# Kernel tuning notes

Hardware: AMD Instinct MI355X
Metric: run time of the kernel (lower is better)

Reference implementation:

```python
import jax, jax.numpy as jnp
import numpy as np

def setup_inputs() -> dict:
    key = jax.random.key(0)
    k1, k2 = jax.random.split(key)
    N, M, D = 4096, 4096, 1024
    set1 = jax.random.normal(k1, (N, D), dtype=jnp.float32)
    set2 = jax.random.normal(k2, (M, D), dtype=jnp.float32)
    return {"set1": set1, "set2": set2}

def _l2_dist(x, y):
    # mean over D of squared differences, computed via the expanded GEMM form
    D = x.shape[-1]
    x2 = jnp.sum(x * x, axis=-1)          # [N]
    y2 = jnp.sum(y * y, axis=-1)          # [M]
    xy = jnp.einsum('nd,md->nm', x, y)    # [N, M]
    return (x2[:, None] - 2.0 * xy + y2[None, :]) / D

def reference(set1, set2):
    dist = _l2_dist(set1, set2)                 # [N, M]
    t1 = jnp.mean(jnp.min(dist, axis=1))        # nearest set2 point per set1 point
    t2 = jnp.mean(jnp.min(dist, axis=0))        # nearest set1 point per set2 point
    return (t1 + t2) * 0.5
```

## Files before the change

kernel.cpp:

```cpp
#include <hip/hip_runtime.h>
#include <hip/hip_bf16.h>
#include <stdint.h>


#define NPTS 4096
#define MPTS 4096
#define DDIM 1024

typedef __attribute__((ext_vector_type(8))) short bf16x8;
typedef __attribute__((ext_vector_type(4))) float f32x4;

__device__ __forceinline__ unsigned short f2bf(float f) {
    unsigned int u = __float_as_uint(f);
    unsigned int r = 0x7FFFu + ((u >> 16) & 1u);
    return (unsigned short)((u + r) >> 16);
}

__device__ __forceinline__ void gl_lds16(const void* g, void* l) {
    __builtin_amdgcn_global_load_lds(
        (const __attribute__((address_space(1))) unsigned int*)g,
        (__attribute__((address_space(3))) unsigned int*)l, 16, 0, 0);
}

__global__ __launch_bounds__(256) void prepass_kernel(
    const float* __restrict__ s1, const float* __restrict__ s2,
    unsigned short* __restrict__ b1, unsigned short* __restrict__ b2,
    float* __restrict__ norms ) {
    int row = blockIdx.x;
    const float* src;
    unsigned short* dst;
    if (row < NPTS) { src = s1 + (size_t)row * DDIM; dst = b1 + (size_t)row * DDIM; }
    else            { src = s2 + (size_t)(row - NPTS) * DDIM; dst = b2 + (size_t)(row - NPTS) * DDIM; }
    int t = threadIdx.x;
    float4 v = ((const float4*)src)[t];
    float sq = v.x * v.x + v.y * v.y + v.z * v.z + v.w * v.w;
    ushort4 o;
    o.x = f2bf(v.x); o.y = f2bf(v.y); o.z = f2bf(v.z); o.w = f2bf(v.w);
    ((ushort4*)dst)[t] = o;
    #pragma unroll
    for (int off = 32; off; off >>= 1) sq += __shfl_down(sq, off, 64);
    __shared__ float red[4];
    if ((t & 63) == 0) red[t >> 6] = sq;
    __syncthreads();
    if (t == 0) norms[row] = red[0] + red[1] + red[2] + red[3];
}

#define BM 128
#define BN 128
#define BK 64

__global__ __launch_bounds__(256) void cham_gemm_kernel(
    const unsigned short* __restrict__ A,
    const unsigned short* __restrict__ B,
    const float* __restrict__ x2, const float* __restrict__ y2,
    unsigned int* __restrict__ rowmin, unsigned int* __restrict__ colmin) {
    __shared__ unsigned short As[BM][BK];
    __shared__ unsigned short Bs[BN][BK];

    const int bid = blockIdx.x;
    const int bi = bid >> 5;
    const int bj = bid & 31;
    const int tid = threadIdx.x;
    const int wave = tid >> 6;
    const int lane = tid & 63;
    const int wr = wave >> 1;
    const int wc = wave & 1;

    f32x4 acc[4][4];
    #pragma unroll
    for (int i = 0; i < 4; ++i)
        #pragma unroll
        for (int j = 0; j < 4; ++j)
            acc[i][j] = (f32x4){0.f, 0.f, 0.f, 0.f};

    const unsigned short* Ab = A + (size_t)(bi * BM) * DDIM;
    const unsigned short* Bb = B + (size_t)(bj * BN) * DDIM;
    const char* AsB = (const char*)&As[0][0];
    const char* BsB = (const char*)&Bs[0][0];

    const int lr = lane >> 3;
    const int ch = lane & 7;

    for (int k0 = 0; k0 < DDIM; k0 += BK) {
        #pragma unroll
        for (int q = 0; q < 4; ++q) {
            int r = wave * 32 + q * 8 + lr;
            int sch = ch ^ (r & 7);
            gl_lds16(Ab + (size_t)r * DDIM + k0 + sch * 8, (void*)&As[wave * 32 + q * 8][0]);
            gl_lds16(Bb + (size_t)r * DDIM + k0 + sch * 8, (void*)&Bs[wave * 32 + q * 8][0]);
        }
        __syncthreads();

        #pragma unroll
        for (int kk = 0; kk < 2; ++kk) {
            const int kb = kk * 32 + (lane >> 4) * 8;
            bf16x8 af[4], bfr[4];
            #pragma unroll
            for (int fi = 0; fi < 4; ++fi) {
                int row = wr * 64 + fi * 16 + (lane & 15);
                int off = row * (BK * 2) + kb * 2;
                af[fi] = *(const bf16x8*)(AsB + (off ^ ((row & 7) << 4)));
            }
            #pragma unroll
            for (int fj = 0; fj < 4; ++fj) {
                int col = wc * 64 + fj * 16 + (lane & 15);
                int off = col * (BK * 2) + kb * 2;
                bfr[fj] = *(const bf16x8*)(BsB + (off ^ ((col & 7) << 4)));
            }
            #pragma unroll
            for (int fi = 0; fi < 4; ++fi)
                #pragma unroll
                for (int fj = 0; fj < 4; ++fj)
                    acc[fi][fj] = __builtin_amdgcn_mfma_f32_16x16x32_bf16(
                        af[fi], bfr[fj], acc[fi][fj], 0, 0, 0);
        }
        __syncthreads();
    }

    const float invD = 1.0f / (float)DDIM;
    const int nb = bi * BM + wr * 64;
    const int mb = bj * BN + wc * 64;

    float x2v[4][4];
    #pragma unroll
    for (int fi = 0; fi < 4; ++fi)
        #pragma unroll
        for (int rg = 0; rg < 4; ++rg)
            x2v[fi][rg] = x2[nb + fi * 16 + (lane >> 4) * 4 + rg];
    float y2v[4];
    #pragma unroll
    for (int fj = 0; fj < 4; ++fj)
        y2v[fj] = y2[mb + fj * 16 + (lane & 15)];

    float rv[4][4];
    float cv[4];
    #pragma unroll
    for (int fi = 0; fi < 4; ++fi)
        #pragma unroll
        for (int rg = 0; rg < 4; ++rg) rv[fi][rg] = 3.0e38f;
    #pragma unroll
    for (int fj = 0; fj < 4; ++fj) cv[fj] = 3.0e38f;

    #pragma unroll
    for (int fi = 0; fi < 4; ++fi)
        #pragma unroll
        for (int fj = 0; fj < 4; ++fj)
            #pragma unroll
            for (int rg = 0; rg < 4; ++rg) {
                float d = (x2v[fi][rg] + y2v[fj] - 2.0f * acc[fi][fj][rg]) * invD;
                rv[fi][rg] = fminf(rv[fi][rg], d);
                cv[fj] = fminf(cv[fj], d);
            }

    #pragma unroll
    for (int fi = 0; fi < 4; ++fi)
        #pragma unroll
        for (int rg = 0; rg < 4; ++rg) {
            float v = rv[fi][rg];
            v = fminf(v, __shfl_xor(v, 1, 64));
            v = fminf(v, __shfl_xor(v, 2, 64));
            v = fminf(v, __shfl_xor(v, 4, 64));
            v = fminf(v, __shfl_xor(v, 8, 64));
            if ((lane & 15) == 0) {
                int n = nb + fi * 16 + (lane >> 4) * 4 + rg;
                atomicMin(&rowmin[n], __float_as_uint(v));
            }
        }

    #pragma unroll
    for (int fj = 0; fj < 4; ++fj) {
        float v = cv[fj];
        v = fminf(v, __shfl_xor(v, 16, 64));
        v = fminf(v, __shfl_xor(v, 32, 64));
        if (lane < 16) {
            int m = mb + fj * 16 + lane;
            atomicMin(&colmin[m], __float_as_uint(v));
        }
    }
}

__global__ __launch_bounds__(1024) void finredux_kernel(
    const unsigned int* __restrict__ mins , float* __restrict__ out) {
    int t = threadIdx.x;
    float s = 0.f;
    #pragma unroll
    for (int i = 0; i < 8; ++i) s += __uint_as_float(mins[t + i * 1024]);
    #pragma unroll
    for (int off = 32; off; off >>= 1) s += __shfl_down(s, off, 64);
    __shared__ float ws_[16];
    if ((t & 63) == 0) ws_[t >> 6] = s;
    __syncthreads();
    if (t == 0) {
        float tot = 0.f;
        #pragma unroll
        for (int i = 0; i < 16; ++i) tot += ws_[i];
        out[0] = tot * (1.0f / 8192.0f);
    }
}

extern "C" void kernel_launch(void* const* d_in, const int* in_sizes, int n_in,
                              void* d_out, int out_size, void* d_ws, size_t ws_size,
                              hipStream_t stream) {
    const float* s1 = (const float*)d_in[0];
    const float* s2 = (const float*)d_in[1];
    char* ws = (char*)d_ws;

    unsigned short* b1 = (unsigned short*)ws;
    unsigned short* b2 = (unsigned short*)(ws + 8388608);
    float* norms       = (float*)(ws + 16777216);
    unsigned int* mins = (unsigned int*)(ws + 16777216 + 32768);
    float* out = (float*)d_out;

    hipMemsetAsync(mins, 0x7f, 32768, stream);

    prepass_kernel<<<NPTS + MPTS, 256, 0, stream>>>(s1, s2, b1, b2, norms);
    cham_gemm_kernel<<<(NPTS / BM) * (MPTS / BN), 256, 0, stream>>>(
        b1, b2, norms, norms + NPTS, mins, mins + NPTS);
    finredux_kernel<<<1, 1024, 0, stream>>>(mins, out);
}
```

Baseline: 130.9 us.

## Use 256x256 tiles with 4-slot async LDS pipeline and fold mins init into prepass

The GEMM moves from 128x128 tiles with 256 threads to 256x256 tiles with 512 threads (8 waves). A 4-slot, 128KB LDS ring buffer is filled by direct global-to-LDS loads issued several stages ahead, with explicit waitcnt, barriers and priority boosts around the MFMA blocks. This aims to hide load latency and raise arithmetic intensity, at the cost of only 256 blocks, which is about one per CU, and heavy register pressure. The prepass now handles one row per wave and initialises the min buffers itself, which removes the separate memset launch.

```diff
diff --git a/kernel.cpp b/kernel.cpp
--- a/kernel.cpp
+++ b/kernel.cpp
@@ -6,6 +6,7 @@
 #define NPTS 4096
 #define MPTS 4096
 #define DDIM 1024
+#define SLOTB 32768
 
 typedef __attribute__((ext_vector_type(8))) short bf16x8;
 typedef __attribute__((ext_vector_type(4))) float f32x4;
@@ -25,157 +26,171 @@
 __global__ __launch_bounds__(256) void prepass_kernel(
     const float* __restrict__ s1, const float* __restrict__ s2,
     unsigned short* __restrict__ b1, unsigned short* __restrict__ b2,
-    float* __restrict__ norms ) {
-    int row = blockIdx.x;
+    float* __restrict__ norms, unsigned int* __restrict__ mins) {
+    const int row = blockIdx.x * 4 + (threadIdx.x >> 6);
+    const int lane = threadIdx.x & 63;
     const float* src;
     unsigned short* dst;
     if (row < NPTS) { src = s1 + (size_t)row * DDIM; dst = b1 + (size_t)row * DDIM; }
     else            { src = s2 + (size_t)(row - NPTS) * DDIM; dst = b2 + (size_t)(row - NPTS) * DDIM; }
-    int t = threadIdx.x;
-    float4 v = ((const float4*)src)[t];
-    float sq = v.x * v.x + v.y * v.y + v.z * v.z + v.w * v.w;
-    ushort4 o;
-    o.x = f2bf(v.x); o.y = f2bf(v.y); o.z = f2bf(v.z); o.w = f2bf(v.w);
-    ((ushort4*)dst)[t] = o;
+    float sq = 0.f;
+    #pragma unroll
+    for (int i = 0; i < 4; ++i) {
+        float4 v = ((const float4*)src)[lane + i * 64];
+        sq += v.x * v.x + v.y * v.y + v.z * v.z + v.w * v.w;
+        ushort4 o;
+        o.x = f2bf(v.x); o.y = f2bf(v.y); o.z = f2bf(v.z); o.w = f2bf(v.w);
+        ((ushort4*)dst)[lane + i * 64] = o;
+    }
     #pragma unroll
     for (int off = 32; off; off >>= 1) sq += __shfl_down(sq, off, 64);
-    __shared__ float red[4];
-    if ((t & 63) == 0) red[t >> 6] = sq;
-    __syncthreads();
-    if (t == 0) norms[row] = red[0] + red[1] + red[2] + red[3];
-}
-
-#define BM 128
-#define BN 128
-#define BK 64
-
-__global__ __launch_bounds__(256) void cham_gemm_kernel(
+    if (lane == 0) { norms[row] = sq; mins[row] = 0x7f7f7f7fu; }
+}
+
+
+#define STAGE2(u, i0) do {                                                      \
+    if ((u) < 32) {                                                             \
+        const int slot_ = (u) & 3;                                              \
+        const int k0_ = ((u) >> 1) * 64 + ((u) & 1) * 32;                       \
+        _Pragma("unroll")                                                       \
+        for (int ii_ = 0; ii_ < 2; ++ii_) {                                     \
+            const int i_ = (i0) + ii_;                                          \
+            const int row_ = i_ * 64 + wave * 8 + srow_l;                       \
+            const unsigned short* g_ = (sc < 4)                                 \
+                ? (Ab + (size_t)row_ * DDIM + k0_ + sc * 8)                     \
+                : (Bb + (size_t)row_ * DDIM + k0_ + (sc - 4) * 8);              \
+            gl_lds16(g_, ldsb + slot_ * SLOTB + i_ * 8192 + wave * 1024);       \
+        }                                                                       \
+    }                                                                           \
+} while (0)
+
+#define PHASE(slot_, FH, STAGECALL, ENDWAIT) do {                               \
+    bf16x8 af_[4];                                                              \
+    if ((FH) == 0) {                                                            \
+        _Pragma("unroll")                                                       \
+        for (int fj_ = 0; fj_ < 4; ++fj_) {                                     \
+            const int col_ = wc * 64 + fj_ * 16 + r0;                           \
+            bf[fj_] = *(const bf16x8*)(ldsb + (slot_) * SLOTB + col_ * 128 + chunkB); \
+        }                                                                       \
+    }                                                                           \
+    _Pragma("unroll")                                                           \
+    for (int fl_ = 0; fl_ < 4; ++fl_) {                                         \
+        const int arow_ = wr * 128 + (FH) * 64 + fl_ * 16 + r0;                 \
+        af_[fl_] = *(const bf16x8*)(ldsb + (slot_) * SLOTB + arow_ * 128 + chunkA); \
+    }                                                                           \
+    STAGECALL;                                                                  \
+    __builtin_amdgcn_s_barrier();                                               \
+    asm volatile("s_waitcnt lgkmcnt(0)" ::: "memory");                          \
+    __builtin_amdgcn_sched_barrier(0);                                          \
+    __builtin_amdgcn_s_setprio(1);                                              \
+    _Pragma("unroll")                                                           \
+    for (int fl_ = 0; fl_ < 4; ++fl_)                                           \
+        _Pragma("unroll")                                                       \
+        for (int fj_ = 0; fj_ < 4; ++fj_)                                       \
+            acc[(FH) * 4 + fl_][fj_] = __builtin_amdgcn_mfma_f32_16x16x32_bf16( \
+                af_[fl_], bf[fj_], acc[(FH) * 4 + fl_][fj_], 0, 0, 0);          \
+    __builtin_amdgcn_s_setprio(0);                                              \
+    ENDWAIT;                                                                    \
+    __builtin_amdgcn_s_barrier();                                               \
+    __builtin_amdgcn_sched_barrier(0);                                          \
+} while (0)
+
+__global__ __launch_bounds__(512, 2) void cham_gemm_kernel(
     const unsigned short* __restrict__ A,
     const unsigned short* __restrict__ B,
     const float* __restrict__ x2, const float* __restrict__ y2,
     unsigned int* __restrict__ rowmin, unsigned int* __restrict__ colmin) {
-    __shared__ unsigned short As[BM][BK];
-    __shared__ unsigned short Bs[BN][BK];
-
-    const int bid = blockIdx.x;
-    const int bi = bid >> 5;
-    const int bj = bid & 31;
+    __shared__ __align__(16) unsigned short lds_us[65536];
+    char* ldsb = (char*)lds_us;
+
+    const int bi = blockIdx.x & 15;
+    const int bj = blockIdx.x >> 4;
     const int tid = threadIdx.x;
     const int wave = tid >> 6;
     const int lane = tid & 63;
-    const int wr = wave >> 1;
-    const int wc = wave & 1;
-
-    f32x4 acc[4][4];
-    #pragma unroll
-    for (int i = 0; i < 4; ++i)
+    const int wr = wave >> 2;
+    const int wc = wave & 3;
+    const int r0 = lane & 15;
+    const int q = lane >> 4;
+
+    const int chunkA = ((q ^ (r0 & 7)) << 4);
+    const int chunkB = (((4 + q) ^ (r0 & 7)) << 4);
+
+    const int srow_l = lane >> 3;
+    const int sc = (lane & 7) ^ srow_l;
+
+    const unsigned short* Ab = A + (size_t)(bi * 256) * DDIM;
+    const unsigned short* Bb = B + (size_t)(bj * 256) * DDIM;
+
+    f32x4 acc[8][4];
+    #pragma unroll
+    for (int i = 0; i < 8; ++i)
         #pragma unroll
         for (int j = 0; j < 4; ++j)
             acc[i][j] = (f32x4){0.f, 0.f, 0.f, 0.f};
 
-    const unsigned short* Ab = A + (size_t)(bi * BM) * DDIM;
-    const unsigned short* Bb = B + (size_t)(bj * BN) * DDIM;
-    const char* AsB = (const char*)&As[0][0];
-    const char* BsB = (const char*)&Bs[0][0];
-
-    const int lr = lane >> 3;
-    const int ch = lane & 7;
-
-    for (int k0 = 0; k0 < DDIM; k0 += BK) {
+    bf16x8 bf[4];
+
+    STAGE2(0, 0); STAGE2(0, 2);
+    STAGE2(1, 0); STAGE2(1, 2);
+    STAGE2(2, 0); STAGE2(2, 2);
+    asm volatile("s_waitcnt vmcnt(4)" ::: "memory");
+    __builtin_amdgcn_s_barrier();
+    __builtin_amdgcn_sched_barrier(0);
+
+    #pragma unroll 2
+    for (int t = 0; t < 16; ++t) {
+        const int s0 = (2 * t) & 3;
+        const int s1 = (2 * t + 1) & 3;
+        const int u0 = 2 * t + 3;
+        const int u1 = 2 * t + 4;
+        PHASE(s0, 0, STAGE2(u0, 0), );
+        PHASE(s0, 1, STAGE2(u0, 2), );
+        PHASE(s1, 0, STAGE2(u1, 0), );
+        PHASE(s1, 1, STAGE2(u1, 2),
+              if (t == 14) { asm volatile("s_waitcnt vmcnt(0)" ::: "memory"); }
+              else if (t < 14) { asm volatile("s_waitcnt vmcnt(4)" ::: "memory"); });
+    }
+
+    const float invD = 1.0f / (float)DDIM;
+    const int nb = bi * 256 + wr * 128;
+    const int mb = bj * 256 + wc * 64;
+
+    float y2v[4];
+    #pragma unroll
+    for (int fj = 0; fj < 4; ++fj) y2v[fj] = y2[mb + fj * 16 + r0];
+
+    float cv[4];
+    #pragma unroll
+    for (int fj = 0; fj < 4; ++fj) cv[fj] = 3.0e38f;
+
+    #pragma unroll
+    for (int fi = 0; fi < 8; ++fi) {
         #pragma unroll
-        for (int q = 0; q < 4; ++q) {
-            int r = wave * 32 + q * 8 + lr;
-            int sch = ch ^ (r & 7);
-            gl_lds16(Ab + (size_t)r * DDIM + k0 + sch * 8, (void*)&As[wave * 32 + q * 8][0]);
-            gl_lds16(Bb + (size_t)r * DDIM + k0 + sch * 8, (void*)&Bs[wave * 32 + q * 8][0]);
-        }
-        __syncthreads();
-
-        #pragma unroll
-        for (int kk = 0; kk < 2; ++kk) {
-            const int kb = kk * 32 + (lane >> 4) * 8;
-            bf16x8 af[4], bfr[4];
-            #pragma unroll
-            for (int fi = 0; fi < 4; ++fi) {
-                int row = wr * 64 + fi * 16 + (lane & 15);
-                int off = row * (BK * 2) + kb * 2;
-                af[fi] = *(const bf16x8*)(AsB + (off ^ ((row & 7) << 4)));
-            }
+        for (int rg = 0; rg < 4; ++rg) {
+            const int n = nb + fi * 16 + q * 4 + rg;
+            const float x2v = x2[n];
+            float rv = 3.0e38f;
             #pragma unroll
             for (int fj = 0; fj < 4; ++fj) {
-                int col = wc * 64 + fj * 16 + (lane & 15);
-                int off = col * (BK * 2) + kb * 2;
-                bfr[fj] = *(const bf16x8*)(BsB + (off ^ ((col & 7) << 4)));
-            }
-            #pragma unroll
-            for (int fi = 0; fi < 4; ++fi)
-                #pragma unroll
-                for (int fj = 0; fj < 4; ++fj)
-                    acc[fi][fj] = __builtin_amdgcn_mfma_f32_16x16x32_bf16(
-                        af[fi], bfr[fj], acc[fi][fj], 0, 0, 0);
-        }
-        __syncthreads();
-    }
-
-    const float invD = 1.0f / (float)DDIM;
-    const int nb = bi * BM + wr * 64;
-    const int mb = bj * BN + wc * 64;
-
-    float x2v[4][4];
-    #pragma unroll
-    for (int fi = 0; fi < 4; ++fi)
-        #pragma unroll
-        for (int rg = 0; rg < 4; ++rg)
-            x2v[fi][rg] = x2[nb + fi * 16 + (lane >> 4) * 4 + rg];
-    float y2v[4];
-    #pragma unroll
-    for (int fj = 0; fj < 4; ++fj)
-        y2v[fj] = y2[mb + fj * 16 + (lane & 15)];
-
-    float rv[4][4];
-    float cv[4];
-    #pragma unroll
-    for (int fi = 0; fi < 4; ++fi)
-        #pragma unroll
-        for (int rg = 0; rg < 4; ++rg) rv[fi][rg] = 3.0e38f;
-    #pragma unroll
-    for (int fj = 0; fj < 4; ++fj) cv[fj] = 3.0e38f;
-
-    #pragma unroll
-    for (int fi = 0; fi < 4; ++fi)
-        #pragma unroll
-        for (int fj = 0; fj < 4; ++fj)
-            #pragma unroll
-            for (int rg = 0; rg < 4; ++rg) {
-                float d = (x2v[fi][rg] + y2v[fj] - 2.0f * acc[fi][fj][rg]) * invD;
-                rv[fi][rg] = fminf(rv[fi][rg], d);
+                float d = (x2v + y2v[fj] - 2.0f * acc[fi][fj][rg]) * invD;
+                rv = fminf(rv, d);
                 cv[fj] = fminf(cv[fj], d);
             }
-
-    #pragma unroll
-    for (int fi = 0; fi < 4; ++fi)
-        #pragma unroll
-        for (int rg = 0; rg < 4; ++rg) {
-            float v = rv[fi][rg];
-            v = fminf(v, __shfl_xor(v, 1, 64));
-            v = fminf(v, __shfl_xor(v, 2, 64));
-            v = fminf(v, __shfl_xor(v, 4, 64));
-            v = fminf(v, __shfl_xor(v, 8, 64));
-            if ((lane & 15) == 0) {
-                int n = nb + fi * 16 + (lane >> 4) * 4 + rg;
-                atomicMin(&rowmin[n], __float_as_uint(v));
-            }
+            rv = fminf(rv, __shfl_xor(rv, 1, 64));
+            rv = fminf(rv, __shfl_xor(rv, 2, 64));
+            rv = fminf(rv, __shfl_xor(rv, 4, 64));
+            rv = fminf(rv, __shfl_xor(rv, 8, 64));
+            if (r0 == 0) atomicMin(&rowmin[n], __float_as_uint(rv));
         }
+    }
 
     #pragma unroll
     for (int fj = 0; fj < 4; ++fj) {
         float v = cv[fj];
         v = fminf(v, __shfl_xor(v, 16, 64));
         v = fminf(v, __shfl_xor(v, 32, 64));
-        if (lane < 16) {
-            int m = mb + fj * 16 + lane;
-            atomicMin(&colmin[m], __float_as_uint(v));
-        }
+        if (lane < 16) atomicMin(&colmin[mb + fj * 16 + lane], __float_as_uint(v));
     }
 }
 
@@ -211,10 +226,8 @@
     unsigned int* mins = (unsigned int*)(ws + 16777216 + 32768);
     float* out = (float*)d_out;
 
-    hipMemsetAsync(mins, 0x7f, 32768, stream);
-
-    prepass_kernel<<<NPTS + MPTS, 256, 0, stream>>>(s1, s2, b1, b2, norms);
-    cham_gemm_kernel<<<(NPTS / BM) * (MPTS / BN), 256, 0, stream>>>(
-        b1, b2, norms, norms + NPTS, mins, mins + NPTS);
+    prepass_kernel<<<2048, 256, 0, stream>>>(s1, s2, b1, b2, norms, mins);
+    cham_gemm_kernel<<<256, 512, 0, stream>>>(b1, b2, norms, norms + NPTS,
+                                              mins, mins + NPTS);
     finredux_kernel<<<1, 1024, 0, stream>>>(mins, out);
 }
```

After: 151.7 us. 1.16x slower.
